# Optimization experiments

Measured on AMD Instinct MI355X. Metric: run time of the kernel, lower is better.

The kernel has to match this reference:

```python
import jax, jax.numpy as jnp
import numpy as np

B, T, D = 4, 4096, 1024
LN_EPS = 1e-5

def _xavier(key, shape, gain=1.0):
    fan_in, fan_out = shape[1], shape[0]
    a = gain * np.sqrt(6.0 / (fan_in + fan_out))
    return jax.random.uniform(key, shape, jnp.float32, -a, a)

def setup_inputs() -> dict:
    key = jax.random.key(0)
    kx, kg, kv, ko = jax.random.split(key, 4)
    # log_decay param init so that softplus(log_decay) == decay_init (0.01)
    log_decay = jnp.asarray(np.log(np.expm1(0.01)), jnp.float32)
    return {
        "x": jax.random.normal(kx, (B, T, D), jnp.float32),
        "ln_w": jnp.ones((D,), jnp.float32),
        "ln_b": jnp.zeros((D,), jnp.float32),
        "gate_w": _xavier(kg, (D, D)),            # torch Linear weight [out, in]
        "gate_b": jnp.zeros((D,), jnp.float32),
        "value_w": _xavier(kv, (D, D), gain=0.01),
        "value_b": jnp.zeros((D,), jnp.float32),
        "out_w": _xavier(ko, (D, D), gain=0.01),
        "out_b": jnp.zeros((D,), jnp.float32),
        "log_decay": log_decay,
    }

def reference(x, ln_w, ln_b, gate_w, gate_b, value_w, value_b, out_w, out_b, log_decay):
    # LayerNorm over last dim
    mu = jnp.mean(x, axis=-1, keepdims=True)
    var = jnp.mean(jnp.square(x - mu), axis=-1, keepdims=True)
    normed = (x - mu) * jax.lax.rsqrt(var + LN_EPS) * ln_w + ln_b
    # gate / value projections (torch Linear: y = x @ W.T + b)
    g = jax.nn.sigmoid(normed @ gate_w.T + gate_b)
    v = normed @ value_w.T + value_b
    # push-pull: cumsum(g*v) - cumsum((1-g)*v) == cumsum((2g-1)*v)
    cumsum = jnp.cumsum((2.0 * g - 1.0) * v, axis=1)
    alpha = jax.nn.softplus(log_decay)
    positions = jnp.arange(T, dtype=jnp.float32)
    decay = jnp.exp(-alpha * positions)[None, :, None]  # [1, T, 1]
    output = cumsum * decay
    return x + (output @ out_w.T + out_b)
```

## Files before the change

### kernel.cpp

```cpp
#include <hip/hip_runtime.h>
#include <hip/hip_bf16.h>

#define BB 4
#define TT 4096
#define DD 1024
#define MM (BB * TT)
#define LN_EPS 1e-5f

typedef __attribute__((ext_vector_type(8))) short bf16x8;
typedef __attribute__((ext_vector_type(4))) float f32x4;

__device__ __forceinline__ float bfbits2f(unsigned short h) {
    return __uint_as_float(((unsigned int)h) << 16);
}
__device__ __forceinline__ unsigned short f2bfbits(float f) {
    __hip_bfloat16 h = __float2bfloat16(f);
    return *reinterpret_cast<unsigned short*>(&h);
}

__device__ __forceinline__ void async_copy16(void* lds, const void* g) {
    __builtin_amdgcn_global_load_lds(
        (const __attribute__((address_space(1))) void*)g,
        (__attribute__((address_space(3))) void*)lds,
        16, 0, 0);
}

__global__ __launch_bounds__(256)
void convert_w(const float* __restrict__ src, __hip_bfloat16* __restrict__ dst)
{
    const size_t i = ((size_t)blockIdx.x * 256 + threadIdx.x) * 4;
    float4 v = *(const float4*)(src + i);
    ushort4 o;
    o.x = f2bfbits(v.x);
    o.y = f2bfbits(v.y);
    o.z = f2bfbits(v.z);
    o.w = f2bfbits(v.w);
    *(ushort4*)((unsigned short*)dst + i) = o;
}

__global__ __launch_bounds__(256)
void ln_kernel(const float* __restrict__ x,
               const float* __restrict__ w,
               const float* __restrict__ b,
               __hip_bfloat16* __restrict__ out)
{
    const int row = blockIdx.x;
    const int tid = threadIdx.x;

    float4 v = *(const float4*)(x + (size_t)row * DD + tid * 4);

    float s  = v.x + v.y + v.z + v.w;
    float ss = fmaf(v.x, v.x, fmaf(v.y, v.y, fmaf(v.z, v.z, v.w * v.w)));

    #pragma unroll
    for (int o = 32; o > 0; o >>= 1) {
        s  += __shfl_down(s, o);
        ss += __shfl_down(ss, o);
    }

    __shared__ float red[8];
    const int wave = tid >> 6, lane = tid & 63;
    if (lane == 0) { red[wave] = s; red[4 + wave] = ss; }
    __syncthreads();
    s  = red[0] + red[1] + red[2] + red[3];
    ss = red[4] + red[5] + red[6] + red[7];

    const float mu   = s * (1.0f / DD);
    const float var  = ss * (1.0f / DD) - mu * mu;
    const float rstd = rsqrtf(var + LN_EPS);

    float4 wr = *(const float4*)(w + tid * 4);
    float4 br = *(const float4*)(b + tid * 4);

    ushort4 o4;
    o4.x = f2bfbits((v.x - mu) * rstd * wr.x + br.x);
    o4.y = f2bfbits((v.y - mu) * rstd * wr.y + br.y);
    o4.z = f2bfbits((v.z - mu) * rstd * wr.z + br.z);
    o4.w = f2bfbits((v.w - mu) * rstd * wr.w + br.w);
    *(ushort4*)((unsigned short*)out + (size_t)row * DD + tid * 4) = o4;
}

__global__ __launch_bounds__(256, 2)
void dual_gemm_gate(const __hip_bfloat16* __restrict__ A,
                    const __hip_bfloat16* __restrict__ Wg,
                    const __hip_bfloat16* __restrict__ Wv,
                    const float* __restrict__ gb,
                    const float* __restrict__ vb,
                    __hip_bfloat16* __restrict__ U,
                    int M, int N, int K)
{
    constexpr int BK = 32;
    __shared__ short As[128 * BK];
    __shared__ short Bg[128 * BK];
    __shared__ short Bv[128 * BK];

    const int tid  = threadIdx.x;
    const int m0   = blockIdx.x * 128;
    const int n0   = blockIdx.y * 128;
    const int wave = tid >> 6;
    const int lane = tid & 63;
    const int wm   = (wave & 1) * 64;
    const int wn   = (wave >> 1) * 64;
    const int lrow = lane & 15;
    const int kgrp = lane >> 4;

    f32x4 accg[4][4] = {};
    f32x4 accv[4][4] = {};

    const int srow = tid >> 2;
    const int sc   = tid & 3;
    const __hip_bfloat16* ga0 = A  + (size_t)(m0 + srow) * K + sc * 8;
    const __hip_bfloat16* gg0 = Wg + (size_t)(n0 + srow) * K + sc * 8;
    const __hip_bfloat16* gv0 = Wv + (size_t)(n0 + srow) * K + sc * 8;

    for (int k0 = 0; k0 < K; k0 += BK) {
        #pragma unroll
        for (int r = 0; r < 2; ++r) {
            async_copy16(&As[(r * 256 + tid) * 8], ga0 + (size_t)r * 64 * K + k0);
            async_copy16(&Bg[(r * 256 + tid) * 8], gg0 + (size_t)r * 64 * K + k0);
            async_copy16(&Bv[(r * 256 + tid) * 8], gv0 + (size_t)r * 64 * K + k0);
        }
        __builtin_amdgcn_s_waitcnt(0);
        __syncthreads();

        bf16x8 af[4], bgf[4], bvf[4];
        #pragma unroll
        for (int i = 0; i < 4; ++i)
            af[i] = *(const bf16x8*)&As[(wm + i * 16 + lrow) * BK + kgrp * 8];
        #pragma unroll
        for (int j = 0; j < 4; ++j) {
            bgf[j] = *(const bf16x8*)&Bg[(wn + j * 16 + lrow) * BK + kgrp * 8];
            bvf[j] = *(const bf16x8*)&Bv[(wn + j * 16 + lrow) * BK + kgrp * 8];
        }

        #pragma unroll
        for (int i = 0; i < 4; ++i)
            #pragma unroll
            for (int j = 0; j < 4; ++j) {
                accg[i][j] = __builtin_amdgcn_mfma_f32_16x16x32_bf16(
                    af[i], bgf[j], accg[i][j], 0, 0, 0);
                accv[i][j] = __builtin_amdgcn_mfma_f32_16x16x32_bf16(
                    af[i], bvf[j], accv[i][j], 0, 0, 0);
            }
        __syncthreads();
    }

    #pragma unroll
    for (int j = 0; j < 4; ++j) {
        const int col = n0 + wn + j * 16 + lrow;
        const float gbv = gb[col];
        const float vbv = vb[col];
        #pragma unroll
        for (int i = 0; i < 4; ++i) {
            #pragma unroll
            for (int r = 0; r < 4; ++r) {
                const int row = m0 + wm + i * 16 + kgrp * 4 + r;
                const float g = accg[i][j][r] + gbv;
                const float v = accv[i][j][r] + vbv;
                const float u = (2.0f / (1.0f + __expf(-g)) - 1.0f) * v;
                U[(size_t)row * N + col] = __float2bfloat16(u);
            }
        }
    }
}

__global__ __launch_bounds__(256, 2)
void gemm_out(const __hip_bfloat16* __restrict__ A,
              const __hip_bfloat16* __restrict__ W,
              const float* __restrict__ bias,
              const float* __restrict__ X,
              float* __restrict__ C,
              int M, int N, int K)
{
    constexpr int BK = 32;
    __shared__ short As[128 * BK];
    __shared__ short Bs[128 * BK];

    const int tid  = threadIdx.x;
    const int m0   = blockIdx.x * 128;
    const int n0   = blockIdx.y * 128;
    const int wave = tid >> 6;
    const int lane = tid & 63;
    const int wm   = (wave & 1) * 64;
    const int wn   = (wave >> 1) * 64;
    const int lrow = lane & 15;
    const int kgrp = lane >> 4;

    f32x4 acc[4][4] = {};

    const int srow = tid >> 2;
    const int sc   = tid & 3;
    const __hip_bfloat16* ga0 = A + (size_t)(m0 + srow) * K + sc * 8;
    const __hip_bfloat16* gb0 = W + (size_t)(n0 + srow) * K + sc * 8;

    for (int k0 = 0; k0 < K; k0 += BK) {
        #pragma unroll
        for (int r = 0; r < 2; ++r) {
            async_copy16(&As[(r * 256 + tid) * 8], ga0 + (size_t)r * 64 * K + k0);
            async_copy16(&Bs[(r * 256 + tid) * 8], gb0 + (size_t)r * 64 * K + k0);
        }
        __builtin_amdgcn_s_waitcnt(0);
        __syncthreads();

        bf16x8 af[4], bfr[4];
        #pragma unroll
        for (int i = 0; i < 4; ++i)
            af[i] = *(const bf16x8*)&As[(wm + i * 16 + lrow) * BK + kgrp * 8];
        #pragma unroll
        for (int j = 0; j < 4; ++j)
            bfr[j] = *(const bf16x8*)&Bs[(wn + j * 16 + lrow) * BK + kgrp * 8];

        #pragma unroll
        for (int i = 0; i < 4; ++i)
            #pragma unroll
            for (int j = 0; j < 4; ++j)
                acc[i][j] = __builtin_amdgcn_mfma_f32_16x16x32_bf16(
                    af[i], bfr[j], acc[i][j], 0, 0, 0);
        __syncthreads();
    }

    #pragma unroll
    for (int j = 0; j < 4; ++j) {
        const int col = n0 + wn + j * 16 + lrow;
        const float bv = bias[col];
        #pragma unroll
        for (int i = 0; i < 4; ++i) {
            #pragma unroll
            for (int r = 0; r < 4; ++r) {
                const int row = m0 + wm + i * 16 + kgrp * 4 + r;
                const size_t idx = (size_t)row * N + col;
                C[idx] = acc[i][j][r] + bv + X[idx];
            }
        }
    }
}

#define NC 64
#define CL 64

__global__ __launch_bounds__(256)
void scan_partial(const __hip_bfloat16* __restrict__ U, float* __restrict__ Pk)
{
    const int c = blockIdx.x, b = blockIdx.y;
    const int d4 = threadIdx.x * 4;
    const unsigned short* p = (const unsigned short*)U +
        ((size_t)b * TT + (size_t)c * CL) * DD + d4;
    float s0 = 0, s1 = 0, s2 = 0, s3 = 0;
    #pragma unroll 16
    for (int t = 0; t < CL; ++t) {
        uint2 raw = *(const uint2*)(p + (size_t)t * DD);
        s0 += bfbits2f((unsigned short)(raw.x & 0xFFFF));
        s1 += bfbits2f((unsigned short)(raw.x >> 16));
        s2 += bfbits2f((unsigned short)(raw.y & 0xFFFF));
        s3 += bfbits2f((unsigned short)(raw.y >> 16));
    }
    *(float4*)&Pk[((size_t)b * NC + c) * DD + d4] = make_float4(s0, s1, s2, s3);
}

__global__ __launch_bounds__(256)
void scan_offsets(float* __restrict__ Pk)
{
    const int col4 = ((int)blockIdx.x * 256 + (int)threadIdx.x) * 4;
    const int b = col4 >> 10;
    const int d = col4 & 1023;
    float r0 = 0, r1 = 0, r2 = 0, r3 = 0;
    float* p = Pk + (size_t)b * NC * DD + d;
    #pragma unroll 8
    for (int c = 0; c < NC; ++c) {
        float4 v = *(float4*)(p + (size_t)c * DD);
        *(float4*)(p + (size_t)c * DD) = make_float4(r0, r1, r2, r3);
        r0 += v.x; r1 += v.y; r2 += v.z; r3 += v.w;
    }
}

__global__ __launch_bounds__(256)
void scan_final(const __hip_bfloat16* __restrict__ U,
                const float* __restrict__ Pk,
                const float* __restrict__ log_decay,
                __hip_bfloat16* __restrict__ S)
{
    const int c = blockIdx.x, b = blockIdx.y;
    const int d4 = threadIdx.x * 4;

    const float ld = log_decay[0];
    const float alpha = log1pf(__expf(ld));
    const float ratio = __expf(-alpha);
    float dec = __expf(-alpha * (float)(c * CL));

    float4 run = *(const float4*)&Pk[((size_t)b * NC + c) * DD + d4];
    const size_t base = ((size_t)b * TT + (size_t)c * CL) * DD + d4;
    const unsigned short* up = (const unsigned short*)U + base;
    unsigned short* sp = (unsigned short*)S + base;

    #pragma unroll 16
    for (int t = 0; t < CL; ++t) {
        uint2 raw = *(const uint2*)(up + (size_t)t * DD);
        run.x += bfbits2f((unsigned short)(raw.x & 0xFFFF));
        run.y += bfbits2f((unsigned short)(raw.x >> 16));
        run.z += bfbits2f((unsigned short)(raw.y & 0xFFFF));
        run.w += bfbits2f((unsigned short)(raw.y >> 16));
        uint2 o;
        o.x = (unsigned int)f2bfbits(run.x * dec) |
              ((unsigned int)f2bfbits(run.y * dec) << 16);
        o.y = (unsigned int)f2bfbits(run.z * dec) |
              ((unsigned int)f2bfbits(run.w * dec) << 16);
        *(uint2*)(sp + (size_t)t * DD) = o;
        dec *= ratio;
    }
}

extern "C" void kernel_launch(void* const* d_in, const int* in_sizes, int n_in,
                              void* d_out, int out_size, void* d_ws, size_t ws_size,
                              hipStream_t stream)
{
    const float* x        = (const float*)d_in[0];
    const float* ln_w     = (const float*)d_in[1];
    const float* ln_b     = (const float*)d_in[2];
    const float* gate_w   = (const float*)d_in[3];
    const float* gate_b   = (const float*)d_in[4];
    const float* value_w  = (const float*)d_in[5];
    const float* value_b  = (const float*)d_in[6];
    const float* out_w    = (const float*)d_in[7];
    const float* out_b    = (const float*)d_in[8];
    const float* log_dec  = (const float*)d_in[9];
    float* out = (float*)d_out;

    char* ws = (char*)d_ws;
    const size_t MB = 1024 * 1024;
    __hip_bfloat16* normed = (__hip_bfloat16*)(ws);
    __hip_bfloat16* S      = (__hip_bfloat16*)(ws);
    float*          Pk     = (float*)(ws + 32 * MB);
    __hip_bfloat16* Wg16   = (__hip_bfloat16*)(ws + 33 * MB);
    __hip_bfloat16* Wv16   = (__hip_bfloat16*)(ws + 35 * MB);
    __hip_bfloat16* Wo16   = (__hip_bfloat16*)(ws + 37 * MB);
    __hip_bfloat16* U      = (__hip_bfloat16*)d_out;

    convert_w<<<dim3(1024), dim3(256), 0, stream>>>(gate_w,  Wg16);
    convert_w<<<dim3(1024), dim3(256), 0, stream>>>(value_w, Wv16);
    convert_w<<<dim3(1024), dim3(256), 0, stream>>>(out_w,   Wo16);

    ln_kernel<<<dim3(MM), dim3(256), 0, stream>>>(x, ln_w, ln_b, normed);

    dual_gemm_gate<<<dim3(MM / 128, DD / 128), dim3(256), 0, stream>>>(
        normed, Wg16, Wv16, gate_b, value_b, U, MM, DD, DD);

    scan_partial<<<dim3(NC, BB), dim3(256), 0, stream>>>(U, Pk);
    scan_offsets<<<dim3(4), dim3(256), 0, stream>>>(Pk);
    scan_final<<<dim3(NC, BB), dim3(256), 0, stream>>>(U, Pk, log_dec, S);

    gemm_out<<<dim3(MM / 128, DD / 128), dim3(256), 0, stream>>>(
        S, Wo16, out_b, x, out, MM, DD, DD);
}
```

Before: 316.6 us.

## Vectorize GEMM epilogues via swapped MFMA operands, fuse weight converts, widen LN/scan

Swaps the MFMA A/B operands so each lane holds four consecutive output columns, which lets the gate and out-GEMM epilogues write with packed uint2/float4 stores and read the residual as float4 instead of scattered scalar accesses. The three weight conversions are merged into one launch. LayerNorm now handles one row per wavefront with shuffle-only reduction. The scan kernels use 8-wide bf16 loads with 128-thread blocks. The scan changes halve the thread count per block, which could reduce latency hiding in those kernels.

Measured after the change: 319.6 us. Within noise of the previous version (+0.9%).

```diff
diff --git a/kernel.cpp b/kernel.cpp
--- a/kernel.cpp
+++ b/kernel.cpp
@@ -17,6 +17,9 @@
     __hip_bfloat16 h = __float2bfloat16(f);
     return *reinterpret_cast<unsigned short*>(&h);
 }
+__device__ __forceinline__ unsigned int pack2(float a, float b) {
+    return (unsigned int)f2bfbits(a) | ((unsigned int)f2bfbits(b) << 16);
+}
 
 __device__ __forceinline__ void async_copy16(void* lds, const void* g) {
     __builtin_amdgcn_global_load_lds(
@@ -26,16 +29,21 @@
 }
 
 __global__ __launch_bounds__(256)
-void convert_w(const float* __restrict__ src, __hip_bfloat16* __restrict__ dst)
-{
-    const size_t i = ((size_t)blockIdx.x * 256 + threadIdx.x) * 4;
+void convert_w3(const float* __restrict__ s0, const float* __restrict__ s1,
+                const float* __restrict__ s2,
+                __hip_bfloat16* __restrict__ d0, __hip_bfloat16* __restrict__ d1,
+                __hip_bfloat16* __restrict__ d2)
+{
+    const int blk = blockIdx.x;
+    const int w = blk >> 10;
+    const float* src = (w == 0) ? s0 : (w == 1) ? s1 : s2;
+    __hip_bfloat16* dst = (w == 0) ? d0 : (w == 1) ? d1 : d2;
+    const size_t i = ((size_t)(blk & 1023) * 256 + threadIdx.x) * 4;
     float4 v = *(const float4*)(src + i);
-    ushort4 o;
-    o.x = f2bfbits(v.x);
-    o.y = f2bfbits(v.y);
-    o.z = f2bfbits(v.z);
-    o.w = f2bfbits(v.w);
-    *(ushort4*)((unsigned short*)dst + i) = o;
+    uint2 o;
+    o.x = pack2(v.x, v.y);
+    o.y = pack2(v.z, v.w);
+    *(uint2*)((unsigned short*)dst + i) = o;
 }
 
 __global__ __launch_bounds__(256)
@@ -44,40 +52,49 @@
                const float* __restrict__ b,
                __hip_bfloat16* __restrict__ out)
 {
-    const int row = blockIdx.x;
-    const int tid = threadIdx.x;
-
-    float4 v = *(const float4*)(x + (size_t)row * DD + tid * 4);
-
-    float s  = v.x + v.y + v.z + v.w;
-    float ss = fmaf(v.x, v.x, fmaf(v.y, v.y, fmaf(v.z, v.z, v.w * v.w)));
-
+    const int wv   = threadIdx.x >> 6;
+    const int lane = threadIdx.x & 63;
+    const int row  = blockIdx.x * 4 + wv;
+
+    const float* xr = x + (size_t)row * DD + lane * 16;
+    float4 v[4];
+    #pragma unroll
+    for (int i = 0; i < 4; ++i) v[i] = *(const float4*)(xr + i * 4);
+
+    float s = 0.0f, ss = 0.0f;
+    #pragma unroll
+    for (int i = 0; i < 4; ++i) {
+        s  += (v[i].x + v[i].y) + (v[i].z + v[i].w);
+        ss += fmaf(v[i].x, v[i].x, fmaf(v[i].y, v[i].y,
+              fmaf(v[i].z, v[i].z, v[i].w * v[i].w)));
+    }
     #pragma unroll
     for (int o = 32; o > 0; o >>= 1) {
         s  += __shfl_down(s, o);
         ss += __shfl_down(ss, o);
     }
-
-    __shared__ float red[8];
-    const int wave = tid >> 6, lane = tid & 63;
-    if (lane == 0) { red[wave] = s; red[4 + wave] = ss; }
-    __syncthreads();
-    s  = red[0] + red[1] + red[2] + red[3];
-    ss = red[4] + red[5] + red[6] + red[7];
+    s  = __shfl(s, 0);
+    ss = __shfl(ss, 0);
 
     const float mu   = s * (1.0f / DD);
     const float var  = ss * (1.0f / DD) - mu * mu;
     const float rstd = rsqrtf(var + LN_EPS);
 
-    float4 wr = *(const float4*)(w + tid * 4);
-    float4 br = *(const float4*)(b + tid * 4);
-
-    ushort4 o4;
-    o4.x = f2bfbits((v.x - mu) * rstd * wr.x + br.x);
-    o4.y = f2bfbits((v.y - mu) * rstd * wr.y + br.y);
-    o4.z = f2bfbits((v.z - mu) * rstd * wr.z + br.z);
-    o4.w = f2bfbits((v.w - mu) * rstd * wr.w + br.w);
-    *(ushort4*)((unsigned short*)out + (size_t)row * DD + tid * 4) = o4;
+    unsigned int res[8];
+    #pragma unroll
+    for (int i = 0; i < 4; ++i) {
+        float4 wr = *(const float4*)(w + lane * 16 + i * 4);
+        float4 br = *(const float4*)(b + lane * 16 + i * 4);
+        float o0 = (v[i].x - mu) * rstd * wr.x + br.x;
+        float o1 = (v[i].y - mu) * rstd * wr.y + br.y;
+        float o2 = (v[i].z - mu) * rstd * wr.z + br.z;
+        float o3 = (v[i].w - mu) * rstd * wr.w + br.w;
+        res[i * 2]     = pack2(o0, o1);
+        res[i * 2 + 1] = pack2(o2, o3);
+    }
+    unsigned short* op = (unsigned short*)out + (size_t)row * DD + lane * 16;
+    *(uint4*)op       = make_uint4(res[0], res[1], res[2], res[3]);
+    *(uint4*)(op + 8) = make_uint4(res[4], res[5], res[6], res[7]);
 }
 
 __global__ __launch_bounds__(256, 2)
@@ -138,28 +155,33 @@
             #pragma unroll
             for (int j = 0; j < 4; ++j) {
                 accg[i][j] = __builtin_amdgcn_mfma_f32_16x16x32_bf16(
-                    af[i], bgf[j], accg[i][j], 0, 0, 0);
+                    bgf[j], af[i], accg[i][j], 0, 0, 0);
                 accv[i][j] = __builtin_amdgcn_mfma_f32_16x16x32_bf16(
-                    af[i], bvf[j], accv[i][j], 0, 0, 0);
+                    bvf[j], af[i], accv[i][j], 0, 0, 0);
             }
         __syncthreads();
     }
 
     #pragma unroll
     for (int j = 0; j < 4; ++j) {
-        const int col = n0 + wn + j * 16 + lrow;
-        const float gbv = gb[col];
-        const float vbv = vb[col];
+        const int nb = n0 + wn + j * 16 + kgrp * 4;
+        const float4 gb4 = *(const float4*)(gb + nb);
+        const float4 vb4 = *(const float4*)(vb + nb);
         #pragma unroll
         for (int i = 0; i < 4; ++i) {
-            #pragma unroll
-            for (int r = 0; r < 4; ++r) {
-                const int row = m0 + wm + i * 16 + kgrp * 4 + r;
-                const float g = accg[i][j][r] + gbv;
-                const float v = accv[i][j][r] + vbv;
-                const float u = (2.0f / (1.0f + __expf(-g)) - 1.0f) * v;
-                U[(size_t)row * N + col] = __float2bfloat16(u);
-            }
+            const int m = m0 + wm + i * 16 + lrow;
+            const float g0 = accg[i][j][0] + gb4.x, v0 = accv[i][j][0] + vb4.x;
+            const float g1 = accg[i][j][1] + gb4.y, v1 = accv[i][j][1] + vb4.y;
+            const float g2 = accg[i][j][2] + gb4.z, v2 = accv[i][j][2] + vb4.z;
+            const float g3 = accg[i][j][3] + gb4.w, v3 = accv[i][j][3] + vb4.w;
+            const float u0 = (2.0f / (1.0f + __expf(-g0)) - 1.0f) * v0;
+            const float u1 = (2.0f / (1.0f + __expf(-g1)) - 1.0f) * v1;
+            const float u2 = (2.0f / (1.0f + __expf(-g2)) - 1.0f) * v2;
+            const float u3 = (2.0f / (1.0f + __expf(-g3)) - 1.0f) * v3;
+            uint2 o;
+            o.x = pack2(u0, u1);
+            o.y = pack2(u2, u3);
+            *(uint2*)((unsigned short*)U + (size_t)m * N + nb) = o;
         }
     }
 }
@@ -215,22 +237,25 @@
             #pragma unroll
             for (int j = 0; j < 4; ++j)
                 acc[i][j] = __builtin_amdgcn_mfma_f32_16x16x32_bf16(
-                    af[i], bfr[j], acc[i][j], 0, 0, 0);
+                    bfr[j], af[i], acc[i][j], 0, 0, 0);
         __syncthreads();
     }
 
     #pragma unroll
     for (int j = 0; j < 4; ++j) {
-        const int col = n0 + wn + j * 16 + lrow;
-        const float bv = bias[col];
+        const int nb = n0 + wn + j * 16 + kgrp * 4;
+        const float4 bv = *(const float4*)(bias + nb);
         #pragma unroll
         for (int i = 0; i < 4; ++i) {
-            #pragma unroll
-            for (int r = 0; r < 4; ++r) {
-                const int row = m0 + wm + i * 16 + kgrp * 4 + r;
-                const size_t idx = (size_t)row * N + col;
-                C[idx] = acc[i][j][r] + bv + X[idx];
-            }
+            const int m = m0 + wm + i * 16 + lrow;
+            const size_t idx = (size_t)m * N + nb;
+            const float4 xv = *(const float4*)(X + idx);
+            float4 o;
+            o.x = acc[i][j][0] + bv.x + xv.x;
+            o.y = acc[i][j][1] + bv.y + xv.y;
+            o.z = acc[i][j][2] + bv.z + xv.z;
+            o.w = acc[i][j][3] + bv.w + xv.w;
+            *(float4*)(C + idx) = o;
         }
     }
 }
@@ -238,23 +263,27 @@
 #define NC 64
 #define CL 64
 
-__global__ __launch_bounds__(256)
+__global__ __launch_bounds__(128)
 void scan_partial(const __hip_bfloat16* __restrict__ U, float* __restrict__ Pk)
 {
     const int c = blockIdx.x, b = blockIdx.y;
-    const int d4 = threadIdx.x * 4;
+    const int d8 = threadIdx.x * 8;
     const unsigned short* p = (const unsigned short*)U +
-        ((size_t)b * TT + (size_t)c * CL) * DD + d4;
-    float s0 = 0, s1 = 0, s2 = 0, s3 = 0;
-    #pragma unroll 16
+        ((size_t)b * TT + (size_t)c * CL) * DD + d8;
+    float s[8] = {};
+    #pragma unroll 8
     for (int t = 0; t < CL; ++t) {
-        uint2 raw = *(const uint2*)(p + (size_t)t * DD);
-        s0 += bfbits2f((unsigned short)(raw.x & 0xFFFF));
-        s1 += bfbits2f((unsigned short)(raw.x >> 16));
-        s2 += bfbits2f((unsigned short)(raw.y & 0xFFFF));
-        s3 += bfbits2f((unsigned short)(raw.y >> 16));
-    }
-    *(float4*)&Pk[((size_t)b * NC + c) * DD + d4] = make_float4(s0, s1, s2, s3);
+        uint4 raw = *(const uint4*)(p + (size_t)t * DD);
+        unsigned int wds[4] = {raw.x, raw.y, raw.z, raw.w};
+        #pragma unroll
+        for (int k = 0; k < 4; ++k) {
+            s[2 * k]     += bfbits2f((unsigned short)(wds[k] & 0xFFFF));
+            s[2 * k + 1] += bfbits2f((unsigned short)(wds[k] >> 16));
+        }
+    }
+    float* o = &Pk[((size_t)b * NC + c) * DD + d8];
+    *(float4*)o       = make_float4(s[0], s[1], s[2], s[3]);
+    *(float4*)(o + 4) = make_float4(s[4], s[5], s[6], s[7]);
 }
 
 __global__ __launch_bounds__(256)
@@ -273,38 +302,44 @@
     }
 }
 
-__global__ __launch_bounds__(256)
+__global__ __launch_bounds__(128)
 void scan_final(const __hip_bfloat16* __restrict__ U,
                 const float* __restrict__ Pk,
                 const float* __restrict__ log_decay,
                 __hip_bfloat16* __restrict__ S)
 {
     const int c = blockIdx.x, b = blockIdx.y;
-    const int d4 = threadIdx.x * 4;
+    const int d8 = threadIdx.x * 8;
 
     const float ld = log_decay[0];
     const float alpha = log1pf(__expf(ld));
     const float ratio = __expf(-alpha);
     float dec = __expf(-alpha * (float)(c * CL));
 
-    float4 run = *(const float4*)&Pk[((size_t)b * NC + c) * DD + d4];
-    const size_t base = ((size_t)b * TT + (size_t)c * CL) * DD + d4;
+    const float* pk = &Pk[((size_t)b * NC + c) * DD + d8];
+    float run[8];
+    float4 r0 = *(const float4*)pk;
+    float4 r1 = *(const float4*)(pk + 4);
+    run[0] = r0.x; run[1] = r0.y; run[2] = r0.z; run[3] = r0.w;
+    run[4] = r1.x; run[5] = r1.y; run[6] = r1.z; run[7] = r1.w;
+
+    const size_t base = ((size_t)b * TT + (size_t)c * CL) * DD + d8;
     const unsigned short* up = (const unsigned short*)U + base;
     unsigned short* sp = (unsigned short*)S + base;
 
-    #pragma unroll 16
+    #pragma unroll 8
     for (int t = 0; t < CL; ++t) {
-        uint2 raw = *(const uint2*)(up + (size_t)t * DD);
-        run.x += bfbits2f((unsigned short)(raw.x & 0xFFFF));
-        run.y += bfbits2f((unsigned short)(raw.x >> 16));
-        run.z += bfbits2f((unsigned short)(raw.y & 0xFFFF));
-        run.w += bfbits2f((unsigned short)(raw.y >> 16));
-        uint2 o;
-        o.x = (unsigned int)f2bfbits(run.x * dec) |
-              ((unsigned int)f2bfbits(run.y * dec) << 16);
-        o.y = (unsigned int)f2bfbits(run.z * dec) |
-              ((unsigned int)f2bfbits(run.w * dec) << 16);
-        *(uint2*)(sp + (size_t)t * DD) = o;
+        uint4 raw = *(const uint4*)(up + (size_t)t * DD);
+        unsigned int wds[4] = {raw.x, raw.y, raw.z, raw.w};
+        uint4 o;
+        unsigned int* ow = (unsigned int*)&o;
+        #pragma unroll
+        for (int k = 0; k < 4; ++k) {
+            run[2 * k]     += bfbits2f((unsigned short)(wds[k] & 0xFFFF));
+            run[2 * k + 1] += bfbits2f((unsigned short)(wds[k] >> 16));
+            ow[k] = pack2(run[2 * k] * dec, run[2 * k + 1] * dec);
+        }
+        *(uint4*)(sp + (size_t)t * DD) = o;
         dec *= ratio;
     }
 }
@@ -335,18 +370,17 @@
     __hip_bfloat16* Wo16   = (__hip_bfloat16*)(ws + 37 * MB);
     __hip_bfloat16* U      = (__hip_bfloat16*)d_out;
 
-    convert_w<<<dim3(1024), dim3(256), 0, stream>>>(gate_w,  Wg16);
-    convert_w<<<dim3(1024), dim3(256), 0, stream>>>(value_w, Wv16);
-    convert_w<<<dim3(1024), dim3(256), 0, stream>>>(out_w,   Wo16);
-
-    ln_kernel<<<dim3(MM), dim3(256), 0, stream>>>(x, ln_w, ln_b, normed);
+    convert_w3<<<dim3(3072), dim3(256), 0, stream>>>(
+        gate_w, value_w, out_w, Wg16, Wv16, Wo16);
+
+    ln_kernel<<<dim3(MM / 4), dim3(256), 0, stream>>>(x, ln_w, ln_b, normed);
 
     dual_gemm_gate<<<dim3(MM / 128, DD / 128), dim3(256), 0, stream>>>(
         normed, Wg16, Wv16, gate_b, value_b, U, MM, DD, DD);
 
-    scan_partial<<<dim3(NC, BB), dim3(256), 0, stream>>>(U, Pk);
+    scan_partial<<<dim3(NC, BB), dim3(128), 0, stream>>>(U, Pk);
     scan_offsets<<<dim3(4), dim3(256), 0, stream>>>(Pk);
-    scan_final<<<dim3(NC, BB), dim3(256), 0, stream>>>(U, Pk, log_dec, S);
+    scan_final<<<dim3(NC, BB), dim3(128), 0, stream>>>(U, Pk, log_dec, S);
 
     gemm_out<<<dim3(MM / 128, DD / 128), dim3(256), 0, stream>>>(
         S, Wo16, out_b, x, out, MM, DD, DD);
```
